# Kernel tuning notes

Hardware: AMD Instinct MI355X
Metric: run time of the kernel (lower is better)

Reference implementation:

```python
import jax, jax.numpy as jnp
import numpy as np

# --- constants from params (see init_kwargs) ---
DY = 3
KNOT_DT = 0.1
CLEARANCE = 0.5
MAX_VEL = 3.0
MAX_ACC = 6.0
LAM_S = 1.0
LAM_C = 10.0
LAM_F = 1.0
OPT_LR = 0.01
B, NCP, NOBS = 32, 512, 256


def setup_inputs() -> dict:
    key = jax.random.key(0)
    k1, k2, k3, k4 = jax.random.split(key, 4)
    control_pts = jax.random.normal(k1, (B, NCP * DY), dtype=jnp.float32)
    obs_loc = jax.random.normal(k2, (B, NOBS, DY), dtype=jnp.float32)
    # obstacle ellipsoid semi-axes: strictly positive, in [0.5, 1.0)
    obs_size = jax.random.uniform(k3, (B, NOBS, DY), dtype=jnp.float32) * 0.5 + 0.5
    reference_pts = jax.random.normal(k4, (B, NCP, DY), dtype=jnp.float32)
    return {"t": 0, "control_pts": control_pts, "obs_loc": obs_loc,
            "obs_size": obs_size, "reference_pts": reference_pts}


def _forward(control_pts, obs_loc, obs_size, reference_pts):
    bs = control_pts.shape[0]
    cp = control_pts.reshape(bs, -1, DY)                       # (B, N, Dy)

    # --- update(): direction + intersection with ellipsoid obstacles ---
    diff = reference_pts[:, :, None, :] - obs_loc[:, None, :, :]  # (B, N, O, Dy)
    direction = diff / jnp.linalg.norm(diff, axis=-1, keepdims=True)
    os_ = obs_size[:, None, :, :]                               # (B, 1, O, Dy)
    tt = 1.0 / jnp.sqrt(jnp.sum(direction ** 2 / os_ ** 2, axis=-1, keepdims=True))
    intersection = obs_loc[:, None] + tt * direction            # (B, N, O, Dy)

    # --- smoothness gradient ---
    vel = cp[:, 1:] - cp[:, :-1]
    acc = vel[:, 1:] - vel[:, :-1]
    jerk = acc[:, 1:] - acc[:, :-1]
    sg = jnp.zeros_like(cp)
    sg = sg.at[:, :-3].add(-2.0 * jerk)
    sg = sg.at[:, 1:-2].add(6.0 * jerk)
    sg = sg.at[:, 2:-1].add(-6.0 * jerk)
    sg = sg.at[:, 3:].add(2.0 * jerk)
    sg = sg / bs

    # --- collision gradient (mask + reduce over obstacles) ---
    dist = jnp.sum((cp[:, :, None, :] - intersection) * direction, axis=-1)  # (B, N, O)
    de = CLEARANCE - dist
    a, b = 3.0 * CLEARANCE, -3.0 * CLEARANCE ** 2
    m1 = (de > 0) & (de <= CLEARANCE)
    m2 = de > CLEARANCE
    coef = jnp.where(m1, -3.0 * de ** 2, 0.0) + jnp.where(m2, -(2.0 * a * de + b), 0.0)
    cg = jnp.sum(coef[..., None] * direction, axis=2) / bs      # (B, N, Dy)

    # --- feasibility gradient ---
    velk = jnp.abs(vel / KNOT_DT)
    acck = jnp.abs(acc / KNOT_DT ** 2)
    gv = jnp.where(velk >= MAX_VEL, 2.0 * (velk - MAX_VEL) / KNOT_DT, 0.0)
    vfg = jnp.zeros_like(cp)
    vfg = vfg.at[:, :-1].add(-gv)
    vfg = vfg.at[:, 1:].add(gv)
    ga = jnp.where(acck >= MAX_ACC, 2.0 * (acck - MAX_ACC) / KNOT_DT ** 2, 0.0)
    afg = jnp.zeros_like(cp)
    afg = afg.at[:, :-2].add(ga)
    afg = afg.at[:, 1:-1].add(-2.0 * ga)
    afg = afg.at[:, 2:].add(ga)
    fg = vfg / KNOT_DT ** 2 + afg

    grad = LAM_S * sg + LAM_C * cg + LAM_F * fg
    return (-OPT_LR) * grad.reshape(bs, -1)


def reference(t, control_pts, obs_loc, obs_size, reference_pts):
    return _forward(control_pts, obs_loc, obs_size, reference_pts)
```

## Files before the change

### kernel.cpp

```cpp
#include <hip/hip_runtime.h>

#define NCP   512
#define NOBS  256
#define NB    32
#define DY    3
#define PTS   16
#define GRP   16


__global__ __launch_bounds__(256) void traj_grad_kernel(
    const float* __restrict__ cp,
    const float* __restrict__ obs_loc,
    const float* __restrict__ obs_size,
    const float* __restrict__ ref,
    float* __restrict__ out)
{
    __shared__ float s_ox[NOBS], s_oy[NOBS], s_oz[NOBS];
    __shared__ float s_ia[NOBS], s_ib[NOBS], s_ic[NOBS];

    const int b   = blockIdx.y;
    const int tid = threadIdx.x;

    {
        const int o = tid;
        const float* ol = obs_loc  + ((size_t)b * NOBS + o) * 3;
        const float* os = obs_size + ((size_t)b * NOBS + o) * 3;
        float ox = ol[0], oy = ol[1], oz = ol[2];
        float sx = os[0], sy = os[1], sz = os[2];
        s_ox[o] = ox; s_oy[o] = oy; s_oz[o] = oz;
        s_ia[o] = 1.0f / (sx * sx);
        s_ib[o] = 1.0f / (sy * sy);
        s_ic[o] = 1.0f / (sz * sz);
    }
    __syncthreads();

    const int p = tid >> 4;
    const int g = tid & (GRP - 1);
    const int i = blockIdx.x * PTS + p;

    const float* rp  = ref + ((size_t)b * NCP + i) * 3;
    const float  rx = rp[0], ry = rp[1], rz = rp[2];
    const float* cpi = cp + ((size_t)b * NCP + i) * 3;
    const float  cx = cpi[0], cy = cpi[1], cz = cpi[2];

    float gx = 0.0f, gy = 0.0f, gz = 0.0f;
    #pragma unroll
    for (int k = 0; k < 16; ++k) {
        const int o = (g << 4) | ((k + g) & 15);
        const float ox = s_ox[o], oy = s_oy[o], oz = s_oz[o];
        const float dx = rx - ox, dy = ry - oy, dz = rz - oz;
        const float n2 = dx * dx + dy * dy + dz * dz;
        const float inv_n = rsqrtf(n2);
        const float ux = dx * inv_n, uy = dy * inv_n, uz = dz * inv_n;
        const float s  = ux * ux * s_ia[o] + uy * uy * s_ib[o] + uz * uz * s_ic[o];
        const float tt = rsqrtf(s);
        const float dot = (cx - ox) * ux + (cy - oy) * uy + (cz - oz) * uz;
        const float de  = 0.5f - (dot - tt);
        const float coef = (de > 0.5f) ? (0.75f - 3.0f * de)
                         : ((de > 0.0f) ? (-3.0f * de * de) : 0.0f);
        gx = fmaf(coef, ux, gx);
        gy = fmaf(coef, uy, gy);
        gz = fmaf(coef, uz, gz);
    }

    #pragma unroll
    for (int m = 1; m < GRP; m <<= 1) {
        gx += __shfl_xor(gx, m);
        gy += __shfl_xor(gy, m);
        gz += __shfl_xor(gz, m);
    }

    if (g < DY) {
        const int c = g;
        const float cgv = (c == 0) ? gx : ((c == 1) ? gy : gz);

        float v[7];
        #pragma unroll
        for (int d = -3; d <= 3; ++d) {
            const int j = i + d;
            v[d + 3] = (j >= 0 && j < NCP) ? cp[((size_t)b * NCP + j) * 3 + c] : 0.0f;
        }

        auto Jv = [&](int j) -> float {
            if (j < 0 || j > NCP - 4) return 0.0f;
            const int x = j - i + 3;
            return v[x + 3] - 3.0f * v[x + 2] + 3.0f * v[x + 1] - v[x];
        };
        const float sgv = -2.0f * Jv(i) + 6.0f * Jv(i - 1)
                        - 6.0f * Jv(i - 2) + 2.0f * Jv(i - 3);

        auto Gv = [&](int j) -> float {
            if (j < 0 || j > NCP - 2) return 0.0f;
            const int x = j - i + 3;
            const float velk = fabsf(v[x + 1] - v[x]) * 10.0f;
            return (velk >= 3.0f) ? 20.0f * (velk - 3.0f) : 0.0f;
        };
        const float vfg = Gv(i - 1) - Gv(i);

        auto Ga = [&](int j) -> float {
            if (j < 0 || j > NCP - 3) return 0.0f;
            const int x = j - i + 3;
            const float acck = fabsf(v[x + 2] - 2.0f * v[x + 1] + v[x]) * 100.0f;
            return (acck >= 6.0f) ? 200.0f * (acck - 6.0f) : 0.0f;
        };
        const float afg = Ga(i) - 2.0f * Ga(i - 1) + Ga(i - 2);

        const float fg = 100.0f * vfg + afg;

        const float grad = sgv * (1.0f / 32.0f)
                         + 10.0f * (cgv * (1.0f / 32.0f))
                         + fg;
        out[((size_t)b * NCP + i) * 3 + c] = -0.01f * grad;
    }
}

extern "C" void kernel_launch(void* const* d_in, const int* in_sizes, int n_in,
                              void* d_out, int out_size, void* d_ws, size_t ws_size,
                              hipStream_t stream) {
    const float* cp       = (const float*)d_in[1];
    const float* obs_loc  = (const float*)d_in[2];
    const float* obs_size = (const float*)d_in[3];
    const float* ref      = (const float*)d_in[4];
    float* out = (float*)d_out;

    dim3 grid(NCP / PTS, NB);
    dim3 block(256);
    traj_grad_kernel<<<grid, block, 0, stream>>>(cp, obs_loc, obs_size, ref, out);
}
```

Before: 67.68 us.

## Remap work so lanes own points and broadcast obstacles via readlane

```diff
diff --git a/kernel.cpp b/kernel.cpp
--- a/kernel.cpp
+++ b/kernel.cpp
@@ -3,114 +3,122 @@
 #define NCP   512
 #define NOBS  256
 #define NB    32
-#define DY    3
-#define PTS   16
-#define GRP   16
 
+__device__ __forceinline__ float rl(float v, int lane) {
+    return __int_as_float(__builtin_amdgcn_readlane(__float_as_int(v), lane));
+}
 
-__global__ __launch_bounds__(256) void traj_grad_kernel(
+__global__ __launch_bounds__(512) void traj_grad_kernel(
     const float* __restrict__ cp,
     const float* __restrict__ obs_loc,
     const float* __restrict__ obs_size,
     const float* __restrict__ ref,
     float* __restrict__ out)
 {
-    __shared__ float s_ox[NOBS], s_oy[NOBS], s_oz[NOBS];
-    __shared__ float s_ia[NOBS], s_ib[NOBS], s_ic[NOBS];
+    __shared__ float4 s_red[8][64];
 
-    const int b   = blockIdx.y;
-    const int tid = threadIdx.x;
+    const int b    = blockIdx.y;
+    const int tid  = threadIdx.x;
+    const int lane = tid & 63;
+    const int wv   = tid >> 6;
 
+    float vox = 0.f, voy = 0.f, voz = 0.f, via = 1.f, vib = 1.f, vic = 1.f;
     {
-        const int o = tid;
-        const float* ol = obs_loc  + ((size_t)b * NOBS + o) * 3;
-        const float* os = obs_size + ((size_t)b * NOBS + o) * 3;
-        float ox = ol[0], oy = ol[1], oz = ol[2];
-        float sx = os[0], sy = os[1], sz = os[2];
-        s_ox[o] = ox; s_oy[o] = oy; s_oz[o] = oz;
-        s_ia[o] = 1.0f / (sx * sx);
-        s_ib[o] = 1.0f / (sy * sy);
-        s_ic[o] = 1.0f / (sz * sz);
+        const int o = wv * 32 + lane;
+        if (lane < 32) {
+            const float* ol = obs_loc  + ((size_t)b * NOBS + o) * 3;
+            const float* os = obs_size + ((size_t)b * NOBS + o) * 3;
+            vox = ol[0]; voy = ol[1]; voz = ol[2];
+            const float sx = os[0], sy = os[1], sz = os[2];
+            via = 1.0f / (sx * sx);
+            vib = 1.0f / (sy * sy);
+            vic = 1.0f / (sz * sz);
+        }
     }
+
+    const int i = blockIdx.x * 64 + lane;
+    const size_t base = ((size_t)b * NCP + i) * 3;
+    const float rx = ref[base], ry = ref[base + 1], rz = ref[base + 2];
+    const float cx = cp[base],  cy = cp[base + 1],  cz = cp[base + 2];
+    const float ex = cx - rx,   ey = cy - ry,       ez = cz - rz;
+
+    float gx = 0.f, gy = 0.f, gz = 0.f;
+    #pragma unroll
+    for (int k = 0; k < 32; ++k) {
+        const float ox = rl(vox, k), oy = rl(voy, k), oz = rl(voz, k);
+        const float ia = rl(via, k), ib = rl(vib, k), ic = rl(vic, k);
+        const float dx = rx - ox, dy = ry - oy, dz = rz - oz;
+        const float dx2 = dx * dx, dy2 = dy * dy, dz2 = dz * dz;
+        const float n2 = dx2 + dy2 + dz2;
+        const float w  = fmaf(dz2, ic, fmaf(dy2, ib, dx2 * ia));
+        const float inv_n = rsqrtf(n2);
+        const float rq    = rsqrtf(w);
+        const float ed = fmaf(ex, dx, fmaf(ey, dy, ez * dz));
+        const float inner = fmaf(-n2, rq, n2 + ed);
+        const float dist  = inv_n * inner;
+        float de = 0.5f - dist;
+        de = fmaxf(de, 0.0f);
+        const float m3  = -3.0f * de;
+        const bool  far_ = de > 0.5f;
+        const float t = far_ ? 1.0f  : de;
+        const float s = far_ ? 0.75f : 0.0f;
+        const float coef = fmaf(m3, t, s);
+        const float cf = coef * inv_n;
+        gx = fmaf(cf, dx, gx);
+        gy = fmaf(cf, dy, gy);
+        gz = fmaf(cf, dz, gz);
+    }
+
+    s_red[wv][lane] = make_float4(gx, gy, gz, 0.f);
     __syncthreads();
 
-    const int p = tid >> 4;
-    const int g = tid & (GRP - 1);
-    const int i = blockIdx.x * PTS + p;
+    if (tid < 192) {
+        const int c  = tid >> 6;
+        const int p  = tid & 63;
+        const int i2 = blockIdx.x * 64 + p;
 
-    const float* rp  = ref + ((size_t)b * NCP + i) * 3;
-    const float  rx = rp[0], ry = rp[1], rz = rp[2];
-    const float* cpi = cp + ((size_t)b * NCP + i) * 3;
-    const float  cx = cpi[0], cy = cpi[1], cz = cpi[2];
-
-    float gx = 0.0f, gy = 0.0f, gz = 0.0f;
-    #pragma unroll
-    for (int k = 0; k < 16; ++k) {
-        const int o = (g << 4) | ((k + g) & 15);
-        const float ox = s_ox[o], oy = s_oy[o], oz = s_oz[o];
-        const float dx = rx - ox, dy = ry - oy, dz = rz - oz;
-        const float n2 = dx * dx + dy * dy + dz * dz;
-        const float inv_n = rsqrtf(n2);
-        const float ux = dx * inv_n, uy = dy * inv_n, uz = dz * inv_n;
-        const float s  = ux * ux * s_ia[o] + uy * uy * s_ib[o] + uz * uz * s_ic[o];
-        const float tt = rsqrtf(s);
-        const float dot = (cx - ox) * ux + (cy - oy) * uy + (cz - oz) * uz;
-        const float de  = 0.5f - (dot - tt);
-        const float coef = (de > 0.5f) ? (0.75f - 3.0f * de)
-                         : ((de > 0.0f) ? (-3.0f * de * de) : 0.0f);
-        gx = fmaf(coef, ux, gx);
-        gy = fmaf(coef, uy, gy);
-        gz = fmaf(coef, uz, gz);
-    }
-
-    #pragma unroll
-    for (int m = 1; m < GRP; m <<= 1) {
-        gx += __shfl_xor(gx, m);
-        gy += __shfl_xor(gy, m);
-        gz += __shfl_xor(gz, m);
-    }
-
-    if (g < DY) {
-        const int c = g;
-        const float cgv = (c == 0) ? gx : ((c == 1) ? gy : gz);
+        float cg = 0.f;
+        #pragma unroll
+        for (int w = 0; w < 8; ++w)
+            cg += ((const float*)&s_red[w][p])[c];
 
         float v[7];
         #pragma unroll
         for (int d = -3; d <= 3; ++d) {
-            const int j = i + d;
-            v[d + 3] = (j >= 0 && j < NCP) ? cp[((size_t)b * NCP + j) * 3 + c] : 0.0f;
+            const int j = i2 + d;
+            v[d + 3] = (j >= 0 && j < NCP) ? cp[((size_t)b * NCP + j) * 3 + c] : 0.f;
         }
 
         auto Jv = [&](int j) -> float {
-            if (j < 0 || j > NCP - 4) return 0.0f;
-            const int x = j - i + 3;
-            return v[x + 3] - 3.0f * v[x + 2] + 3.0f * v[x + 1] - v[x];
+            if (j < 0 || j > NCP - 4) return 0.f;
+            const int x = j - i2 + 3;
+            return v[x + 3] - 3.f * v[x + 2] + 3.f * v[x + 1] - v[x];
         };
-        const float sgv = -2.0f * Jv(i) + 6.0f * Jv(i - 1)
-                        - 6.0f * Jv(i - 2) + 2.0f * Jv(i - 3);
+        const float sgv = -2.f * Jv(i2) + 6.f * Jv(i2 - 1)
+                        - 6.f * Jv(i2 - 2) + 2.f * Jv(i2 - 3);
 
         auto Gv = [&](int j) -> float {
-            if (j < 0 || j > NCP - 2) return 0.0f;
-            const int x = j - i + 3;
-            const float velk = fabsf(v[x + 1] - v[x]) * 10.0f;
-            return (velk >= 3.0f) ? 20.0f * (velk - 3.0f) : 0.0f;
+            if (j < 0 || j > NCP - 2) return 0.f;
+            const int x = j - i2 + 3;
+            const float velk = fabsf(v[x + 1] - v[x]) * 10.f;
+            return (velk >= 3.f) ? 20.f * (velk - 3.f) : 0.f;
         };
-        const float vfg = Gv(i - 1) - Gv(i);
+        const float vfg = Gv(i2 - 1) - Gv(i2);
 
         auto Ga = [&](int j) -> float {
-            if (j < 0 || j > NCP - 3) return 0.0f;
-            const int x = j - i + 3;
-            const float acck = fabsf(v[x + 2] - 2.0f * v[x + 1] + v[x]) * 100.0f;
-            return (acck >= 6.0f) ? 200.0f * (acck - 6.0f) : 0.0f;
+            if (j < 0 || j > NCP - 3) return 0.f;
+            const int x = j - i2 + 3;
+            const float acck = fabsf(v[x + 2] - 2.f * v[x + 1] + v[x]) * 100.f;
+            return (acck >= 6.f) ? 200.f * (acck - 6.f) : 0.f;
         };
-        const float afg = Ga(i) - 2.0f * Ga(i - 1) + Ga(i - 2);
+        const float afg = Ga(i2) - 2.f * Ga(i2 - 1) + Ga(i2 - 2);
 
-        const float fg = 100.0f * vfg + afg;
+        const float fg = 100.f * vfg + afg;
 
-        const float grad = sgv * (1.0f / 32.0f)
-                         + 10.0f * (cgv * (1.0f / 32.0f))
+        const float grad = sgv * (1.f / 32.f)
+                         + 10.f * (cg * (1.f / 32.f))
                          + fg;
-        out[((size_t)b * NCP + i) * 3 + c] = -0.01f * grad;
+        out[((size_t)b * NCP + i2) * 3 + c] = -0.01f * grad;
     }
 }
 
@@ -123,7 +131,7 @@
     const float* ref      = (const float*)d_in[4];
     float* out = (float*)d_out;
 
-    dim3 grid(NCP / PTS, NB);
-    dim3 block(256);
+    dim3 grid(NCP / 64, NB);
+    dim3 block(512);
     traj_grad_kernel<<<grid, block, 0, stream>>>(cp, obs_loc, obs_size, ref, out);
 }
```

Result: no change. 67.05 us (-0.9%).
